# Performance work log

Measured on AMD Instinct MI355X. Metric: run time of the kernel, lower is better.

## Reference

```python
import jax, jax.numpy as jnp
import numpy as np

NUM_AGENTS = 8
D_AGENT = 64  # input_dim_single_agent
INPUT_DIM = NUM_AGENTS * D_AGENT
NORM_TERM = NUM_AGENTS - 1 if NUM_AGENTS > 1 else 1
BATCH = 65536


def setup_inputs() -> dict:
    key = jax.random.key(0)
    k1, k2, k3 = jax.random.split(key, 3)
    x = jax.random.normal(k1, (BATCH, INPUT_DIM), dtype=jnp.float32)
    # original code multiplies hidden_weights by 0.1 (twice-written bug leaves comm unscaled)
    hidden_weights = jax.random.normal(k2, (D_AGENT, D_AGENT), dtype=jnp.float32) * 0.1
    communication_weights = jax.random.normal(k3, (D_AGENT, D_AGENT), dtype=jnp.float32)
    return {"x": x, "hidden_weights": hidden_weights,
            "communication_weights": communication_weights}


def reference(x, hidden_weights, communication_weights):
    # Equivalent to y = tanh(x @ final_mat.T) where final_mat has diagonal
    # [d,d] blocks = hidden_weights and off-diagonal blocks = comm/(A-1).
    B = x.shape[0]
    xb = x.reshape(B, NUM_AGENTS, D_AGENT)          # [B, A, d]
    others = xb.sum(axis=1, keepdims=True) - xb      # sum over other agents
    # F.linear uses weight W with out = x @ W.T, hence 'ed' contraction on d
    y = (jnp.einsum('bad,ed->bae', xb, hidden_weights)
         + jnp.einsum('bad,ed->bae', others, communication_weights) / NORM_TERM)
    return jnp.tanh(y).reshape(B, INPUT_DIM)
```

## Files before the change

### kernel.cpp

```cpp
#include <hip/hip_runtime.h>


typedef _Float16 half8v  __attribute__((ext_vector_type(8)));
typedef float    floatx4 __attribute__((ext_vector_type(4)));

#define WAVES_PER_BLOCK 4

__global__ __launch_bounds__(256, 4)
void comm_kernel(const float* __restrict__ x,
                 const float* __restrict__ Hw,
                 const float* __restrict__ Cw,
                 float* __restrict__ out,
                 int ntiles, int nwaves)
{
    const int tid  = threadIdx.x;
    const int lane = tid & 63;
    const int wave = tid >> 6;
    const int quad = lane >> 4;
    const int l16  = lane & 15;
    const int wgid = blockIdx.x * WAVES_PER_BLOCK + wave;

    half8v bfrag[4][4];
    #pragma unroll
    for (int nt = 0; nt < 4; ++nt) {
        const float* hr = Hw + (nt * 16 + l16) * 64 + quad * 8;
        const float* cr = Cw + (nt * 16 + l16) * 64 + quad * 8;
        float h[16], c[16];
        *reinterpret_cast<float4*>(&h[0])  = *reinterpret_cast<const float4*>(hr);
        *reinterpret_cast<float4*>(&h[4])  = *reinterpret_cast<const float4*>(hr + 4);
        *reinterpret_cast<float4*>(&h[8])  = *reinterpret_cast<const float4*>(hr + 32);
        *reinterpret_cast<float4*>(&h[12]) = *reinterpret_cast<const float4*>(hr + 36);
        *reinterpret_cast<float4*>(&c[0])  = *reinterpret_cast<const float4*>(cr);
        *reinterpret_cast<float4*>(&c[4])  = *reinterpret_cast<const float4*>(cr + 4);
        *reinterpret_cast<float4*>(&c[8])  = *reinterpret_cast<const float4*>(cr + 32);
        *reinterpret_cast<float4*>(&c[12]) = *reinterpret_cast<const float4*>(cr + 36);
        half8v b0, b1, b2, b3;
        #pragma unroll
        for (int j = 0; j < 8; ++j) {
            b0[j] = (_Float16)(h[j]     - c[j]     * (1.0f / 7.0f));
            b1[j] = (_Float16)(h[8 + j] - c[8 + j] * (1.0f / 7.0f));
            b2[j] = (_Float16)(c[j]     * (1.0f / 7.0f));
            b3[j] = (_Float16)(c[8 + j] * (1.0f / 7.0f));
        }
        bfrag[0][nt] = b0; bfrag[1][nt] = b1;
        bfrag[2][nt] = b2; bfrag[3][nt] = b3;
    }

    for (int t = wgid; t < ntiles; t += nwaves) {
        const float* xt = x + (size_t)t * 1024 + l16 * 64 + quad * 8;
        float xf[16];
        *reinterpret_cast<float4*>(&xf[0])  = *reinterpret_cast<const float4*>(xt);
        *reinterpret_cast<float4*>(&xf[4])  = *reinterpret_cast<const float4*>(xt + 4);
        *reinterpret_cast<float4*>(&xf[8])  = *reinterpret_cast<const float4*>(xt + 32);
        *reinterpret_cast<float4*>(&xf[12]) = *reinterpret_cast<const float4*>(xt + 36);

        half8v af0, af1;
        #pragma unroll
        for (int j = 0; j < 8; ++j) {
            af0[j] = (_Float16)xf[j];
            af1[j] = (_Float16)xf[8 + j];
        }

        #pragma unroll
        for (int m = 1; m <= 4; m <<= 1) {
            #pragma unroll
            for (int j = 0; j < 16; ++j)
                xf[j] += __shfl_xor(xf[j], m, 64);
        }
        half8v af2, af3;
        #pragma unroll
        for (int j = 0; j < 8; ++j) {
            af2[j] = (_Float16)xf[j];
            af3[j] = (_Float16)xf[8 + j];
        }

        floatx4 acc[4];
        #pragma unroll
        for (int nt = 0; nt < 4; ++nt) acc[nt] = floatx4{0.f, 0.f, 0.f, 0.f};

        #pragma unroll
        for (int nt = 0; nt < 4; ++nt) {
            acc[nt] = __builtin_amdgcn_mfma_f32_16x16x32_f16(af0, bfrag[0][nt], acc[nt], 0, 0, 0);
            acc[nt] = __builtin_amdgcn_mfma_f32_16x16x32_f16(af1, bfrag[1][nt], acc[nt], 0, 0, 0);
            acc[nt] = __builtin_amdgcn_mfma_f32_16x16x32_f16(af2, bfrag[2][nt], acc[nt], 0, 0, 0);
            acc[nt] = __builtin_amdgcn_mfma_f32_16x16x32_f16(af3, bfrag[3][nt], acc[nt], 0, 0, 0);
        }

        float* o = out + (size_t)t * 1024;
        #pragma unroll
        for (int nt = 0; nt < 4; ++nt) {
            const int e = nt * 16 + l16;
            #pragma unroll
            for (int reg = 0; reg < 4; ++reg) {
                float y = acc[nt][reg];
                y = fminf(10.f, fmaxf(-10.f, y));
                const float tv  = __builtin_amdgcn_exp2f(y * 2.8853900817779268f);
                const float res = (tv - 1.f) * __builtin_amdgcn_rcpf(tv + 1.f);
                o[(quad * 4 + reg) * 64 + e] = res;
            }
        }
    }
}

extern "C" void kernel_launch(void* const* d_in, const int* in_sizes, int n_in,
                              void* d_out, int out_size, void* d_ws, size_t ws_size,
                              hipStream_t stream) {
    const float* x  = (const float*)d_in[0];
    const float* Hw = (const float*)d_in[1];
    const float* Cw = (const float*)d_in[2];
    float* out = (float*)d_out;

    const int rows   = in_sizes[0] / 512;
    const int ntiles = rows * 8 / 16;
    const int blocks = 1024;
    const int nwaves = blocks * WAVES_PER_BLOCK;
    comm_kernel<<<blocks, 256, 0, stream>>>(x, Hw, Cw, out, ntiles, nwaves);
}
```

Measured before the change: 249.1 us.

## Swap MFMA operands for vectorized nontemporal stores, stage weights in LDS

Swaps the MFMA operand order so each lane holds four consecutive output columns, which lets each lane write a float4 with a nontemporal store instead of scalar strided stores. The combined weight matrix is built once per block in LDS rather than in registers per wave. The agent sum is done with packed fp16 butterfly shuffles, and the grid now covers the work exactly with a fixed number of tiles per wave. The risks are extra LDS reads per tile and the lower precision of summing the agents in fp16. The exact-cover grid also assumes ntiles is divisible by 16.

Result: slower. 299.7 us (+20.3%).

```diff
diff --git a/kernel.cpp b/kernel.cpp
--- a/kernel.cpp
+++ b/kernel.cpp
@@ -1,77 +1,77 @@
 #include <hip/hip_runtime.h>
 
 
+typedef _Float16 half4v  __attribute__((ext_vector_type(4)));
 typedef _Float16 half8v  __attribute__((ext_vector_type(8)));
 typedef float    floatx4 __attribute__((ext_vector_type(4)));
 
 #define WAVES_PER_BLOCK 4
+#define TILES_PER_WAVE  4
+#define BSTRIDE 136
 
-__global__ __launch_bounds__(256, 4)
+__device__ __forceinline__ half8v h8_bfly_add(half8v v, int mask) {
+    union { half8v h; int i[4]; } u, r;
+    u.h = v;
+    #pragma unroll
+    for (int k = 0; k < 4; ++k) r.i[k] = __shfl_xor(u.i[k], mask, 64);
+    return v + r.h;
+}
+
+__global__ __launch_bounds__(256, 8)
 void comm_kernel(const float* __restrict__ x,
                  const float* __restrict__ Hw,
                  const float* __restrict__ Cw,
-                 float* __restrict__ out,
-                 int ntiles, int nwaves)
+                 float* __restrict__ out)
 {
+    __shared__ __align__(16) _Float16 augB[64 * BSTRIDE];
+
     const int tid  = threadIdx.x;
     const int lane = tid & 63;
     const int wave = tid >> 6;
     const int quad = lane >> 4;
     const int l16  = lane & 15;
+
+    #pragma unroll
+    for (int i = 0; i < 4; ++i) {
+        const int idx = i * 256 + tid;
+        const int e = idx >> 4;
+        const int k = (idx & 15) << 2;
+        const float4 h = *reinterpret_cast<const float4*>(Hw + e * 64 + k);
+        const float4 c = *reinterpret_cast<const float4*>(Cw + e * 64 + k);
+        half4v m4, c4;
+        m4[0] = (_Float16)(h.x - c.x * (1.0f / 7.0f)); c4[0] = (_Float16)(c.x * (1.0f / 7.0f));
+        m4[1] = (_Float16)(h.y - c.y * (1.0f / 7.0f)); c4[1] = (_Float16)(c.y * (1.0f / 7.0f));
+        m4[2] = (_Float16)(h.z - c.z * (1.0f / 7.0f)); c4[2] = (_Float16)(c.z * (1.0f / 7.0f));
+        m4[3] = (_Float16)(h.w - c.w * (1.0f / 7.0f)); c4[3] = (_Float16)(c.w * (1.0f / 7.0f));
+        *reinterpret_cast<half4v*>(&augB[e * BSTRIDE + k])      = m4;
+        *reinterpret_cast<half4v*>(&augB[e * BSTRIDE + 64 + k]) = c4;
+    }
+    __syncthreads();
+
     const int wgid = blockIdx.x * WAVES_PER_BLOCK + wave;
+    const int t0   = wgid * TILES_PER_WAVE;
 
-    half8v bfrag[4][4];
-    #pragma unroll
-    for (int nt = 0; nt < 4; ++nt) {
-        const float* hr = Hw + (nt * 16 + l16) * 64 + quad * 8;
-        const float* cr = Cw + (nt * 16 + l16) * 64 + quad * 8;
-        float h[16], c[16];
-        *reinterpret_cast<float4*>(&h[0])  = *reinterpret_cast<const float4*>(hr);
-        *reinterpret_cast<float4*>(&h[4])  = *reinterpret_cast<const float4*>(hr + 4);
-        *reinterpret_cast<float4*>(&h[8])  = *reinterpret_cast<const float4*>(hr + 32);
-        *reinterpret_cast<float4*>(&h[12]) = *reinterpret_cast<const float4*>(hr + 36);
-        *reinterpret_cast<float4*>(&c[0])  = *reinterpret_cast<const float4*>(cr);
-        *reinterpret_cast<float4*>(&c[4])  = *reinterpret_cast<const float4*>(cr + 4);
-        *reinterpret_cast<float4*>(&c[8])  = *reinterpret_cast<const float4*>(cr + 32);
-        *reinterpret_cast<float4*>(&c[12]) = *reinterpret_cast<const float4*>(cr + 36);
-        half8v b0, b1, b2, b3;
-        #pragma unroll
-        for (int j = 0; j < 8; ++j) {
-            b0[j] = (_Float16)(h[j]     - c[j]     * (1.0f / 7.0f));
-            b1[j] = (_Float16)(h[8 + j] - c[8 + j] * (1.0f / 7.0f));
-            b2[j] = (_Float16)(c[j]     * (1.0f / 7.0f));
-            b3[j] = (_Float16)(c[8 + j] * (1.0f / 7.0f));
-        }
-        bfrag[0][nt] = b0; bfrag[1][nt] = b1;
-        bfrag[2][nt] = b2; bfrag[3][nt] = b3;
-    }
+    #pragma unroll 1
+    for (int i = 0; i < TILES_PER_WAVE; ++i) {
+        const int t = t0 + i;
 
-    for (int t = wgid; t < ntiles; t += nwaves) {
         const float* xt = x + (size_t)t * 1024 + l16 * 64 + quad * 8;
-        float xf[16];
-        *reinterpret_cast<float4*>(&xf[0])  = *reinterpret_cast<const float4*>(xt);
-        *reinterpret_cast<float4*>(&xf[4])  = *reinterpret_cast<const float4*>(xt + 4);
-        *reinterpret_cast<float4*>(&xf[8])  = *reinterpret_cast<const float4*>(xt + 32);
-        *reinterpret_cast<float4*>(&xf[12]) = *reinterpret_cast<const float4*>(xt + 36);
+        float4 v0 = *reinterpret_cast<const float4*>(xt);
+        float4 v1 = *reinterpret_cast<const float4*>(xt + 4);
+        float4 v2 = *reinterpret_cast<const float4*>(xt + 32);
+        float4 v3 = *reinterpret_cast<const float4*>(xt + 36);
 
-        half8v af0, af1;
-        #pragma unroll
-        for (int j = 0; j < 8; ++j) {
-            af0[j] = (_Float16)xf[j];
-            af1[j] = (_Float16)xf[8 + j];
-        }
+        half8v a0, a1;
+        a0[0]=(_Float16)v0.x; a0[1]=(_Float16)v0.y; a0[2]=(_Float16)v0.z; a0[3]=(_Float16)v0.w;
+        a0[4]=(_Float16)v1.x; a0[5]=(_Float16)v1.y; a0[6]=(_Float16)v1.z; a0[7]=(_Float16)v1.w;
+        a1[0]=(_Float16)v2.x; a1[1]=(_Float16)v2.y; a1[2]=(_Float16)v2.z; a1[3]=(_Float16)v2.w;
+        a1[4]=(_Float16)v3.x; a1[5]=(_Float16)v3.y; a1[6]=(_Float16)v3.z; a1[7]=(_Float16)v3.w;
 
+        half8v s0 = a0, s1 = a1;
         #pragma unroll
         for (int m = 1; m <= 4; m <<= 1) {
-            #pragma unroll
-            for (int j = 0; j < 16; ++j)
-                xf[j] += __shfl_xor(xf[j], m, 64);
-        }
-        half8v af2, af3;
-        #pragma unroll
-        for (int j = 0; j < 8; ++j) {
-            af2[j] = (_Float16)xf[j];
-            af3[j] = (_Float16)xf[8 + j];
+            s0 = h8_bfly_add(s0, m);
+            s1 = h8_bfly_add(s1, m);
         }
 
         floatx4 acc[4];
@@ -80,24 +80,29 @@
 
         #pragma unroll
         for (int nt = 0; nt < 4; ++nt) {
-            acc[nt] = __builtin_amdgcn_mfma_f32_16x16x32_f16(af0, bfrag[0][nt], acc[nt], 0, 0, 0);
-            acc[nt] = __builtin_amdgcn_mfma_f32_16x16x32_f16(af1, bfrag[1][nt], acc[nt], 0, 0, 0);
-            acc[nt] = __builtin_amdgcn_mfma_f32_16x16x32_f16(af2, bfrag[2][nt], acc[nt], 0, 0, 0);
-            acc[nt] = __builtin_amdgcn_mfma_f32_16x16x32_f16(af3, bfrag[3][nt], acc[nt], 0, 0, 0);
+            const _Float16* bp = &augB[(nt * 16 + l16) * BSTRIDE + quad * 8];
+            const half8v b0 = *reinterpret_cast<const half8v*>(bp);
+            const half8v b1 = *reinterpret_cast<const half8v*>(bp + 32);
+            const half8v b2 = *reinterpret_cast<const half8v*>(bp + 64);
+            const half8v b3 = *reinterpret_cast<const half8v*>(bp + 96);
+            acc[nt] = __builtin_amdgcn_mfma_f32_16x16x32_f16(b0, a0, acc[nt], 0, 0, 0);
+            acc[nt] = __builtin_amdgcn_mfma_f32_16x16x32_f16(b1, a1, acc[nt], 0, 0, 0);
+            acc[nt] = __builtin_amdgcn_mfma_f32_16x16x32_f16(b2, s0, acc[nt], 0, 0, 0);
+            acc[nt] = __builtin_amdgcn_mfma_f32_16x16x32_f16(b3, s1, acc[nt], 0, 0, 0);
         }
 
-        float* o = out + (size_t)t * 1024;
+        float* o = out + (size_t)t * 1024 + l16 * 64 + quad * 4;
         #pragma unroll
         for (int nt = 0; nt < 4; ++nt) {
-            const int e = nt * 16 + l16;
+            floatx4 r;
             #pragma unroll
             for (int reg = 0; reg < 4; ++reg) {
                 float y = acc[nt][reg];
                 y = fminf(10.f, fmaxf(-10.f, y));
                 const float tv  = __builtin_amdgcn_exp2f(y * 2.8853900817779268f);
-                const float res = (tv - 1.f) * __builtin_amdgcn_rcpf(tv + 1.f);
-                o[(quad * 4 + reg) * 64 + e] = res;
+                r[reg] = (tv - 1.f) * __builtin_amdgcn_rcpf(tv + 1.f);
             }
+            __builtin_nontemporal_store(r, reinterpret_cast<floatx4*>(o + nt * 16));
         }
     }
 }
@@ -112,7 +117,6 @@
 
     const int rows   = in_sizes[0] / 512;
     const int ntiles = rows * 8 / 16;
-    const int blocks = 1024;
-    const int nwaves = blocks * WAVES_PER_BLOCK;
-    comm_kernel<<<blocks, 256, 0, stream>>>(x, Hw, Cw, out, ntiles, nwaves);
+    const int blocks = ntiles / (WAVES_PER_BLOCK * TILES_PER_WAVE);
+    comm_kernel<<<blocks, 256, 0, stream>>>(x, Hw, Cw, out);
 }
```
